# Performance work log

Measured on AMD Instinct MI355X. Metric: run time of the kernel, lower is better.

The kernel has to match this reference:

```python
import jax, jax.numpy as jnp
import numpy as np

INPUT_DIM = 1024
BOTTLENECK = 256
NUM_Q = 8
CODEBOOK = 1024
COMMIT_W = 0.25

def setup_inputs() -> dict:
    key = jax.random.key(0)
    ks = jax.random.split(key, 10)
    s_in = 1.0 / np.sqrt(INPUT_DIM)
    s_bn = 1.0 / np.sqrt(BOTTLENECK)
    return {
        'x': jax.random.normal(ks[0], (8, 2048, INPUT_DIM), jnp.float32),
        'W_e1': jax.random.uniform(ks[1], (INPUT_DIM, INPUT_DIM), jnp.float32, -s_in, s_in),
        'b_e1': jnp.zeros((INPUT_DIM,), jnp.float32),
        'W_e2': jax.random.uniform(ks[2], (INPUT_DIM, BOTTLENECK), jnp.float32, -s_in, s_in),
        'b_e2': jnp.zeros((BOTTLENECK,), jnp.float32),
        'codebooks': jax.random.normal(ks[3], (NUM_Q, CODEBOOK, BOTTLENECK), jnp.float32),
        'W_d1': jax.random.uniform(ks[4], (BOTTLENECK, INPUT_DIM), jnp.float32, -s_bn, s_bn),
        'b_d1': jnp.zeros((INPUT_DIM,), jnp.float32),
        'W_d2': jax.random.uniform(ks[5], (INPUT_DIM, INPUT_DIM), jnp.float32, -s_in, s_in),
        'b_d2': jnp.zeros((INPUT_DIM,), jnp.float32),
    }

def _gelu(x):
    return jax.nn.gelu(x, approximate=False)  # torch nn.GELU default = exact erf

def _rvq(z_flat, codebooks):
    # z_flat: [N, D]; codebooks: [Q, K, D]
    def step(res, cb):
        # squared L2 distances via expansion: [N, K]
        d2 = (jnp.sum(res * res, -1, keepdims=True)
              - 2.0 * res @ cb.T
              + jnp.sum(cb * cb, -1))
        idx = jnp.argmin(d2, axis=-1)                      # [N]
        q = jax.lax.stop_gradient(jnp.take(cb, idx, 0))    # [N, D] (EMA codebook: no grad)
        closs = jnp.mean((res - q) ** 2)
        return res - q, (idx, q, closs)
    _, (indices, qs, closses) = jax.lax.scan(step, z_flat, codebooks)
    q_total = jnp.sum(qs, axis=0)
    # straight-through estimator
    quantized = z_flat + jax.lax.stop_gradient(q_total - z_flat)
    commitment = COMMIT_W * jnp.mean(closses)
    return quantized, indices, commitment

def reference(x, W_e1, b_e1, W_e2, b_e2, codebooks, W_d1, b_d1, W_d2, b_d2):
    lead = x.shape[:-1]
    z = _gelu(x @ W_e1 + b_e1) @ W_e2 + b_e2               # [..., BOTTLENECK]
    zf = z.reshape(-1, BOTTLENECK)
    qf, indices, commitment = _rvq(zf, codebooks)
    quantized = qf.reshape(*lead, BOTTLENECK)
    indices = indices.reshape(NUM_Q, *lead)
    reconstructed = _gelu(quantized @ W_d1 + b_d1) @ W_d2 + b_d2
    return z, quantized, indices, reconstructed, commitment
```

## Files before the change

### kernel.cpp

```cpp
#include <hip/hip_runtime.h>
#include <math.h>

#define NROWS 16384
#define DIN   1024
#define DBN   256
#define NQ    8
#define NCODE 1024
#define MARGIN 2.0f

#define OFF_Z    0
#define OFF_Q    4194304
#define OFF_IDX  8388608
#define OFF_REC  8519680
#define OFF_COM  25296896

typedef __attribute__((ext_vector_type(8))) short short8v;
typedef __attribute__((ext_vector_type(4))) float f32x4;

__device__ __forceinline__ float gelu_f(float x) {
  return 0.5f * x * (1.0f + erff(x * 0.70710678118654752440f));
}

__device__ __forceinline__ ushort f2b(float x) {
  unsigned u = __float_as_uint(x);
  unsigned r = u + 0x7FFF + ((u >> 16) & 1);
  return (ushort)(r >> 16);
}
__device__ __forceinline__ float b2f(ushort u) {
  return __uint_as_float((unsigned)u << 16);
}
__device__ __forceinline__ void split3(float v, ushort& s1, ushort& s2, ushort& s3) {
  s1 = f2b(v);
  const float r1 = v - b2f(s1);
  s2 = f2b(r1);
  s3 = f2b(r1 - b2f(s2));
}

template<bool GELU, bool TWO>
__global__ __launch_bounds__(256) void gemm6(
    const float* __restrict__ Af,
    const ushort* __restrict__ B1, const ushort* __restrict__ B2,
    const ushort* __restrict__ B3,
    const float* __restrict__ bias,
    float* __restrict__ C0, float* __restrict__ C1,
    int N, int K)
{
  __shared__ char lds[49152];
  char* ldsA1 = lds;
  char* ldsA2 = lds + 8192;
  char* ldsA3 = lds + 16384;
  char* ldsB1 = lds + 24576;
  char* ldsB2 = lds + 32768;
  char* ldsB3 = lds + 40960;
  const int tid = threadIdx.x;
  const int bm = blockIdx.x * 128;
  const int bn = blockIdx.y * 128;
  const int lane = tid & 63;
  const int wid = tid >> 6;
  const int wr = wid >> 1, wc = wid & 1;

  const int srow = tid >> 1;
  const int skh  = tid & 1;
  const float* Ap  = Af + (size_t)(bm + srow) * K + skh * 16;
  const ushort* Bp1 = B1 + (size_t)(bn + srow) * K + skh * 16;
  const ushort* Bp2 = B2 + (size_t)(bn + srow) * K + skh * 16;
  const ushort* Bp3 = B3 + (size_t)(bn + srow) * K + skh * 16;
  const int sswz = (srow & 3) << 4;
  const int sbase = srow * 64 + skh * 32;

  f32x4 acc[4][4];
  #pragma unroll
  for (int m = 0; m < 4; ++m)
    #pragma unroll
    for (int n = 0; n < 4; ++n) acc[m][n] = (f32x4)0.f;

  const int nt = K >> 5;
  for (int t = 0; t < nt; ++t) {
    const int k0 = t << 5;
    __syncthreads();
    #pragma unroll
    for (int jf = 0; jf < 4; ++jf) {
      const float4 v = *(const float4*)(Ap + k0 + jf * 4);
      ushort4 h, md, l;
      split3(v.x, h.x, md.x, l.x);
      split3(v.y, h.y, md.y, l.y);
      split3(v.z, h.z, md.z, l.z);
      split3(v.w, h.w, md.w, l.w);
      const int off = (sbase + jf * 8) ^ sswz;
      *(ushort4*)(ldsA1 + off) = h;
      *(ushort4*)(ldsA2 + off) = md;
      *(ushort4*)(ldsA3 + off) = l;
    }
    #pragma unroll
    for (int j = 0; j < 2; ++j) {
      const int off = (sbase + j * 16) ^ sswz;
      *(uint4*)(ldsB1 + off) = *(const uint4*)(Bp1 + k0 + j * 8);
      *(uint4*)(ldsB2 + off) = *(const uint4*)(Bp2 + k0 + j * 8);
      *(uint4*)(ldsB3 + off) = *(const uint4*)(Bp3 + k0 + j * 8);
    }
    __syncthreads();

    short8v a1[4], a2[4], a3[4], b1[4], b2[4], b3[4];
    #pragma unroll
    for (int m = 0; m < 4; ++m) {
      const int row = wr * 64 + m * 16 + (lane & 15);
      const int off = (row * 64 + ((lane >> 4) << 4)) ^ ((row & 3) << 4);
      a1[m] = *(const short8v*)(ldsA1 + off);
      a2[m] = *(const short8v*)(ldsA2 + off);
      a3[m] = *(const short8v*)(ldsA3 + off);
    }
    #pragma unroll
    for (int n = 0; n < 4; ++n) {
      const int row = wc * 64 + n * 16 + (lane & 15);
      const int off = (row * 64 + ((lane >> 4) << 4)) ^ ((row & 3) << 4);
      b1[n] = *(const short8v*)(ldsB1 + off);
      b2[n] = *(const short8v*)(ldsB2 + off);
      b3[n] = *(const short8v*)(ldsB3 + off);
    }
    #pragma unroll
    for (int m = 0; m < 4; ++m)
      #pragma unroll
      for (int n = 0; n < 4; ++n) {
        f32x4 a = acc[m][n];
        a = __builtin_amdgcn_mfma_f32_16x16x32_bf16(a3[m], b1[n], a, 0, 0, 0);
        a = __builtin_amdgcn_mfma_f32_16x16x32_bf16(a1[m], b3[n], a, 0, 0, 0);
        a = __builtin_amdgcn_mfma_f32_16x16x32_bf16(a2[m], b2[n], a, 0, 0, 0);
        a = __builtin_amdgcn_mfma_f32_16x16x32_bf16(a2[m], b1[n], a, 0, 0, 0);
        a = __builtin_amdgcn_mfma_f32_16x16x32_bf16(a1[m], b2[n], a, 0, 0, 0);
        a = __builtin_amdgcn_mfma_f32_16x16x32_bf16(a1[m], b1[n], a, 0, 0, 0);
        acc[m][n] = a;
      }
  }

  #pragma unroll
  for (int n = 0; n < 4; ++n) {
    const int col = bn + wc * 64 + n * 16 + (lane & 15);
    const float bb = bias[col];
    #pragma unroll
    for (int m = 0; m < 4; ++m) {
      const int row0 = bm + wr * 64 + m * 16 + ((lane >> 4) << 2);
      #pragma unroll
      for (int r = 0; r < 4; ++r) {
        float v = acc[m][n][r] + bb;
        if (GELU) v = gelu_f(v);
        C0[(size_t)(row0 + r) * N + col] = v;
        if (TWO) C1[(size_t)(row0 + r) * N + col] = v;
      }
    }
  }
}

__device__ __forceinline__ void mm_core(
    const ushort* __restrict__ A, const ushort* __restrict__ B,
    int K, int bm, int bn, char* lds, f32x4 acc[4][4])
{
  char* ldsA = lds;
  char* ldsB = lds + 16384;
  const int tid = threadIdx.x;
  const int lane = tid & 63;
  const int wid = tid >> 6;
  const int wr = wid >> 1, wc = wid & 1;

  #pragma unroll
  for (int m = 0; m < 4; ++m)
    #pragma unroll
    for (int n = 0; n < 4; ++n) acc[m][n] = (f32x4)0.f;

  const int nt = K >> 6;
  for (int t = 0; t < nt; ++t) {
    const int k0 = t << 6;
    __syncthreads();
    #pragma unroll
    for (int c = 0; c < 4; ++c) {
      const int id = c * 256 + tid;
      const int row = id >> 3, k8 = id & 7;
      const uint4 va = *(const uint4*)(A + (size_t)(bm + row) * K + k0 + k8 * 8);
      const uint4 vb = *(const uint4*)(B + (size_t)(bn + row) * K + k0 + k8 * 8);
      const int off = (row * 128 + k8 * 16) ^ ((row & 7) << 4);
      *(uint4*)(ldsA + off) = va;
      *(uint4*)(ldsB + off) = vb;
    }
    __syncthreads();
    #pragma unroll
    for (int kk = 0; kk < 2; ++kk) {
      short8v af[4], bfr[4];
      #pragma unroll
      for (int m = 0; m < 4; ++m) {
        const int row = wr * 64 + m * 16 + (lane & 15);
        af[m] = *(const short8v*)(ldsA +
            ((row * 128 + kk * 64 + ((lane >> 4) << 4)) ^ ((row & 7) << 4)));
      }
      #pragma unroll
      for (int n = 0; n < 4; ++n) {
        const int row = wc * 64 + n * 16 + (lane & 15);
        bfr[n] = *(const short8v*)(ldsB +
            ((row * 128 + kk * 64 + ((lane >> 4) << 4)) ^ ((row & 7) << 4)));
      }
      #pragma unroll
      for (int m = 0; m < 4; ++m)
        #pragma unroll
        for (int n = 0; n < 4; ++n)
          acc[m][n] = __builtin_amdgcn_mfma_f32_16x16x32_bf16(
              af[m], bfr[n], acc[m][n], 0, 0, 0);
    }
  }
}

__global__ __launch_bounds__(256) void rvq_screen(
    const ushort* __restrict__ resb, const ushort* __restrict__ cbb,
    const float* __restrict__ cnorm, _Float16* __restrict__ D)
{
  __shared__ char lds[32768];
  f32x4 acc[4][4];
  const int bm = blockIdx.x * 128, bn = blockIdx.y * 128;
  mm_core(resb, cbb, DBN, bm, bn, lds, acc);
  const int lane = threadIdx.x & 63;
  const int wid = threadIdx.x >> 6;
  const int wr = wid >> 1, wc = wid & 1;
  #pragma unroll
  for (int n = 0; n < 4; ++n) {
    const int col = bn + wc * 64 + n * 16 + (lane & 15);
    const float cn = cnorm[col];
    #pragma unroll
    for (int m = 0; m < 4; ++m) {
      const int row0 = bm + wr * 64 + m * 16 + ((lane >> 4) << 2);
      #pragma unroll
      for (int r = 0; r < 4; ++r)
        D[(size_t)(row0 + r) * NCODE + col] = (_Float16)(cn - 2.0f * acc[m][n][r]);
    }
  }
}

template<bool GELU, bool OUTF>
__global__ __launch_bounds__(256) void gemm_bf16(
    const ushort* __restrict__ A, const ushort* __restrict__ Bt,
    const float* __restrict__ bias, float* __restrict__ Cf,
    ushort* __restrict__ Cb, int N, int K)
{
  __shared__ char lds[32768];
  f32x4 acc[4][4];
  const int bm = blockIdx.x * 128, bn = blockIdx.y * 128;
  mm_core(A, Bt, K, bm, bn, lds, acc);
  const int lane = threadIdx.x & 63;
  const int wid = threadIdx.x >> 6;
  const int wr = wid >> 1, wc = wid & 1;
  #pragma unroll
  for (int n = 0; n < 4; ++n) {
    const int col = bn + wc * 64 + n * 16 + (lane & 15);
    const float bb = bias[col];
    #pragma unroll
    for (int m = 0; m < 4; ++m) {
      const int row0 = bm + wr * 64 + m * 16 + ((lane >> 4) << 2);
      #pragma unroll
      for (int r = 0; r < 4; ++r) {
        float v = acc[m][n][r] + bb;
        if (GELU) v = gelu_f(v);
        if (OUTF) Cf[(size_t)(row0 + r) * N + col] = v;
        else      Cb[(size_t)(row0 + r) * N + col] = f2b(v);
      }
    }
  }
}

__global__ __launch_bounds__(256) void cnorm_kernel(
    const float* __restrict__ cb, float* __restrict__ cnorm)
{
  const int code = blockIdx.x * 4 + (threadIdx.x >> 6);
  const int lane = threadIdx.x & 63;
  float4 v = *(const float4*)(cb + (size_t)code * DBN + lane * 4);
  float s = v.x * v.x + v.y * v.y + v.z * v.z + v.w * v.w;
  #pragma unroll
  for (int o = 32; o > 0; o >>= 1) s += __shfl_down(s, o, 64);
  if (lane == 0) cnorm[code] = s;
}

__global__ __launch_bounds__(256) void rvq_rescore(
    const _Float16* __restrict__ D, const float* __restrict__ cb_s,
    const float* __restrict__ cnorm_s,
    float* __restrict__ res, ushort* __restrict__ resb,
    float* __restrict__ idx_out, float* __restrict__ closs_part)
{
  __shared__ int cnt[4];
  __shared__ ushort cand[4][128];
  __shared__ float wsum[4];
  const int w = threadIdx.x >> 6, lane = threadIdx.x & 63;
  const int row = blockIdx.x * 4 + w;
  if (lane == 0) cnt[w] = 0;

  union H8 { uint4 u; _Float16 h[8]; };
  const _Float16* Dr = D + (size_t)row * NCODE + lane * 16;
  H8 a0, a1;
  a0.u = *(const uint4*)(Dr);
  a1.u = *(const uint4*)(Dr + 8);
  float dv[16];
  #pragma unroll
  for (int i = 0; i < 8; ++i) { dv[i] = (float)a0.h[i]; dv[8 + i] = (float)a1.h[i]; }

  float mn = dv[0];
  #pragma unroll
  for (int i = 1; i < 16; ++i) mn = fminf(mn, dv[i]);
  #pragma unroll
  for (int o = 32; o > 0; o >>= 1) mn = fminf(mn, __shfl_xor(mn, o, 64));
  const float thr = mn + MARGIN;

  #pragma unroll
  for (int i = 0; i < 16; ++i)
    if (dv[i] < thr) {
      int p = atomicAdd(&cnt[w], 1);
      if (p < 128) cand[w][p] = (ushort)(lane * 16 + i);
    }
  const int ncand = min(cnt[w], 128);

  const float4 r4 = *(const float4*)(res + (size_t)row * DBN + lane * 4);
  float bestv = INFINITY; int besti = 0x7fffffff;
  for (int c = 0; c < ncand; ++c) {
    const int code = cand[w][c];
    const float4 c4 = *(const float4*)(cb_s + (size_t)code * DBN + lane * 4);
    float d = r4.x * c4.x + r4.y * c4.y + r4.z * c4.z + r4.w * c4.w;
    #pragma unroll
    for (int o = 32; o > 0; o >>= 1) d += __shfl_xor(d, o, 64);
    const float ex = cnorm_s[code] - 2.0f * d;
    if (ex < bestv || (ex == bestv && code < besti)) { bestv = ex; besti = code; }
  }

  const float4 q4 = *(const float4*)(cb_s + (size_t)besti * DBN + lane * 4);
  float4 n4;
  n4.x = r4.x - q4.x; n4.y = r4.y - q4.y; n4.z = r4.z - q4.z; n4.w = r4.w - q4.w;
  *(float4*)(res + (size_t)row * DBN + lane * 4) = n4;
  ushort4 nb;
  nb.x = f2b(n4.x); nb.y = f2b(n4.y); nb.z = f2b(n4.z); nb.w = f2b(n4.w);
  *(ushort4*)(resb + (size_t)row * DBN + lane * 4) = nb;

  float s = n4.x * n4.x + n4.y * n4.y + n4.z * n4.z + n4.w * n4.w;
  #pragma unroll
  for (int o = 32; o > 0; o >>= 1) s += __shfl_xor(s, o, 64);
  if (lane == 0) { wsum[w] = s; idx_out[row] = (float)besti; }
  __syncthreads();
  if (threadIdx.x == 0)
    closs_part[blockIdx.x] = wsum[0] + wsum[1] + wsum[2] + wsum[3];
}

__global__ __launch_bounds__(256) void qfix_gather(
    const float* __restrict__ z, const float* __restrict__ idxf,
    const float* __restrict__ cb, float* __restrict__ q, ushort* __restrict__ qb)
{
  const int w = threadIdx.x >> 6, lane = threadIdx.x & 63;
  const int row = blockIdx.x * 4 + w;
  float4 a; a.x = 0.f; a.y = 0.f; a.z = 0.f; a.w = 0.f;
  #pragma unroll
  for (int s = 0; s < NQ; ++s) {
    const int ix = (int)idxf[(size_t)s * NROWS + row];
    const float4 c4 = *(const float4*)(cb + ((size_t)s * NCODE + ix) * DBN + lane * 4);
    a.x += c4.x; a.y += c4.y; a.z += c4.z; a.w += c4.w;
  }
  const float4 z4 = *(const float4*)(z + (size_t)row * DBN + lane * 4);
  float4 qv;
  qv.x = z4.x + (a.x - z4.x); qv.y = z4.y + (a.y - z4.y);
  qv.z = z4.z + (a.z - z4.z); qv.w = z4.w + (a.w - z4.w);
  *(float4*)(q + (size_t)row * DBN + lane * 4) = qv;
  ushort4 qb4;
  qb4.x = f2b(qv.x); qb4.y = f2b(qv.y); qb4.z = f2b(qv.z); qb4.w = f2b(qv.w);
  *(ushort4*)(qb + (size_t)row * DBN + lane * 4) = qb4;
}

__global__ __launch_bounds__(256) void conv_flat(
    const float* __restrict__ in, ushort* __restrict__ out, int n4)
{
  const int i = blockIdx.x * 256 + threadIdx.x;
  if (i >= n4) return;
  const float4 v = *(const float4*)(in + (size_t)i * 4);
  ushort4 o;
  o.x = f2b(v.x); o.y = f2b(v.y); o.z = f2b(v.z); o.w = f2b(v.w);
  *(ushort4*)(out + (size_t)i * 4) = o;
}

__global__ __launch_bounds__(256) void convT(
    const float* __restrict__ in, ushort* __restrict__ out, int K, int N)
{
  __shared__ float t[32][33];
  const int k0 = blockIdx.x * 32, n0 = blockIdx.y * 32;
  const int tx = threadIdx.x & 31, ty = threadIdx.x >> 5;
  #pragma unroll
  for (int i = 0; i < 32; i += 8)
    t[ty + i][tx] = in[(size_t)(k0 + ty + i) * N + n0 + tx];
  __syncthreads();
  #pragma unroll
  for (int i = 0; i < 32; i += 8)
    out[(size_t)(n0 + ty + i) * K + k0 + tx] = f2b(t[tx][ty + i]);
}

__global__ __launch_bounds__(256) void convT_split3(
    const float* __restrict__ in, ushort* __restrict__ o1,
    ushort* __restrict__ o2, ushort* __restrict__ o3, int K, int N)
{
  __shared__ float t[32][33];
  const int k0 = blockIdx.x * 32, n0 = blockIdx.y * 32;
  const int tx = threadIdx.x & 31, ty = threadIdx.x >> 5;
  #pragma unroll
  for (int i = 0; i < 32; i += 8)
    t[ty + i][tx] = in[(size_t)(k0 + ty + i) * N + n0 + tx];
  __syncthreads();
  #pragma unroll
  for (int i = 0; i < 32; i += 8) {
    const float v = t[tx][ty + i];
    ushort s1, s2, s3;
    split3(v, s1, s2, s3);
    const size_t o = (size_t)(n0 + ty + i) * K + k0 + tx;
    o1[o] = s1; o2[o] = s2; o3[o] = s3;
  }
}

__global__ __launch_bounds__(256) void commit_kernel(
    const float* __restrict__ parts, float* __restrict__ out)
{
  __shared__ float sm[256];
  float s = 0.f;
  for (int i = threadIdx.x; i < NQ * 4096; i += 256) s += parts[i];
  sm[threadIdx.x] = s;
  __syncthreads();
  for (int st = 128; st > 0; st >>= 1) {
    if (threadIdx.x < st) sm[threadIdx.x] += sm[threadIdx.x + st];
    __syncthreads();
  }
  if (threadIdx.x == 0)
    out[0] = 0.25f * sm[0] / (8.0f * 4194304.0f);
}

extern "C" void kernel_launch(void* const* d_in, const int* in_sizes, int n_in,
                              void* d_out, int out_size, void* d_ws, size_t ws_size,
                              hipStream_t stream) {
  (void)in_sizes; (void)n_in; (void)out_size; (void)ws_size;
  const float* x    = (const float*)d_in[0];
  const float* W_e1 = (const float*)d_in[1];
  const float* b_e1 = (const float*)d_in[2];
  const float* W_e2 = (const float*)d_in[3];
  const float* b_e2 = (const float*)d_in[4];
  const float* cb   = (const float*)d_in[5];
  const float* W_d1 = (const float*)d_in[6];
  const float* b_d1 = (const float*)d_in[7];
  const float* W_d2 = (const float*)d_in[8];
  const float* b_d2 = (const float*)d_in[9];

  float* out = (float*)d_out;
  float* z_out   = out + OFF_Z;
  float* q_out   = out + OFF_Q;
  float* idx_out = out + OFF_IDX;
  float* rec_out = out + OFF_REC;
  float* com_out = out + OFF_COM;

  float* ws      = (float*)d_ws;
  float* hidden  = ws;
  float* res     = ws + 16777216;
  float* cnorm   = ws + 20971520;
  float* closs   = ws + 20979712;
  ushort* wtail  = (ushort*)(ws + 21012480);
  ushort* We2T1  = wtail;
  ushort* We2T2  = wtail + 262144;
  ushort* We2T3  = wtail + 524288;
  ushort* Wd1T   = wtail + 786432;
  ushort* Wd2T   = wtail + 1048576;

  ushort* resu   = (ushort*)res;
  ushort* We1T1  = resu;
  ushort* We1T2  = resu + 1048576;
  ushort* We1T3  = resu + 2097152;

  ushort* hregion = (ushort*)d_ws;
  _Float16* Dmat = (_Float16*)hregion;
  ushort* resb   = hregion + 16777216;
  ushort* cbb    = hregion + 20971520;
  ushort* qb     = hregion + 20971520;
  ushort* hidb   = hregion;

  cnorm_kernel<<<2048, 256, 0, stream>>>(cb, cnorm);
  convT_split3<<<dim3(32, 32), 256, 0, stream>>>(W_e1, We1T1, We1T2, We1T3, DIN, DIN);
  convT_split3<<<dim3(32, 8),  256, 0, stream>>>(W_e2, We2T1, We2T2, We2T3, DIN, DBN);
  convT<<<dim3(8, 32),  256, 0, stream>>>(W_d1, Wd1T, DBN, DIN);
  convT<<<dim3(32, 32), 256, 0, stream>>>(W_d2, Wd2T, DIN, DIN);

  gemm6<true,  false><<<dim3(128, 8), 256, 0, stream>>>(
      x, We1T1, We1T2, We1T3, b_e1, hidden, nullptr, DIN, DIN);
  gemm6<false, true ><<<dim3(128, 2), 256, 0, stream>>>(
      hidden, We2T1, We2T2, We2T3, b_e2, z_out, res, DBN, DIN);

  conv_flat<<<4096, 256, 0, stream>>>(res, resb, 1048576);
  conv_flat<<<2048, 256, 0, stream>>>(cb, cbb, 524288);

  for (int s = 0; s < NQ; ++s) {
    rvq_screen<<<dim3(128, 8), 256, 0, stream>>>(
        resb, cbb + (size_t)s * NCODE * DBN, cnorm + s * NCODE, Dmat);
    rvq_rescore<<<4096, 256, 0, stream>>>(
        Dmat, cb + (size_t)s * NCODE * DBN, cnorm + s * NCODE,
        res, resb, idx_out + (size_t)s * NROWS, closs + s * 4096);
  }

  qfix_gather<<<4096, 256, 0, stream>>>(z_out, idx_out, cb, q_out, qb);

  gemm_bf16<true,  false><<<dim3(128, 8), 256, 0, stream>>>(qb, Wd1T, b_d1, nullptr, hidb, DIN, DBN);
  gemm_bf16<false, true ><<<dim3(128, 8), 256, 0, stream>>>(hidb, Wd2T, b_d2, rec_out, nullptr, DIN, DIN);

  commit_kernel<<<1, 256, 0, stream>>>(closs, com_out);
}
```

Baseline: 706.7 us.

## Interleave split-bf16 LDS tiles, narrow second encoder GEMM tile, fuse bf16 residual output

The three bf16 split planes of A and B now sit interleaved per row in one LDS buffer with an 8-way XOR swizzle. The A split is done on 16 contiguous floats and written as 16-byte vectors. The second encoder GEMM is templated to a 64-column tile so it launches 512 blocks instead of 256, which gives more parallelism on that small-N GEMM. It also writes the bf16 copy of the residual directly, which removes a separate conversion kernel. The trade-off is more A reloads for the narrow tile and extra stores in the epilogue.

```diff
diff --git a/kernel.cpp b/kernel.cpp
--- a/kernel.cpp
+++ b/kernel.cpp
@@ -33,108 +33,126 @@
   s1 = f2b(v);
   const float r1 = v - b2f(s1);
   s2 = f2b(r1);
-  s3 = f2b(r1 - b2f(s2));
-}
-
-template<bool GELU, bool TWO>
+  const float r2 = r1 - b2f(s2);
+  s3 = f2b(r2);
+}
+
+template<bool GELU, int NB, int OUT>
 __global__ __launch_bounds__(256) void gemm6(
     const float* __restrict__ Af,
     const ushort* __restrict__ B1, const ushort* __restrict__ B2,
     const ushort* __restrict__ B3,
     const float* __restrict__ bias,
-    float* __restrict__ C0, float* __restrict__ C1,
+    float* __restrict__ C0, float* __restrict__ C1, ushort* __restrict__ Ob,
     int N, int K)
 {
-  __shared__ char lds[49152];
-  char* ldsA1 = lds;
-  char* ldsA2 = lds + 8192;
-  char* ldsA3 = lds + 16384;
-  char* ldsB1 = lds + 24576;
-  char* ldsB2 = lds + 32768;
-  char* ldsB3 = lds + 40960;
+  constexpr int BN = NB * 32;
+  __shared__ char lds[24576 + BN * 192];
+  char* ldsA = lds;
+  char* ldsB = lds + 24576;
   const int tid = threadIdx.x;
   const int bm = blockIdx.x * 128;
-  const int bn = blockIdx.y * 128;
+  const int bn = blockIdx.y * BN;
   const int lane = tid & 63;
   const int wid = tid >> 6;
   const int wr = wid >> 1, wc = wid & 1;
 
-  const int srow = tid >> 1;
-  const int skh  = tid & 1;
-  const float* Ap  = Af + (size_t)(bm + srow) * K + skh * 16;
-  const ushort* Bp1 = B1 + (size_t)(bn + srow) * K + skh * 16;
-  const ushort* Bp2 = B2 + (size_t)(bn + srow) * K + skh * 16;
-  const ushort* Bp3 = B3 + (size_t)(bn + srow) * K + skh * 16;
-  const int sswz = (srow & 3) << 4;
-  const int sbase = srow * 64 + skh * 32;
-
-  f32x4 acc[4][4];
+  const int srow = tid >> 1, skh = tid & 1;
+  const float* Ap = Af + (size_t)(bm + srow) * K + skh * 16;
+  const int abase = srow * 192;
+  const int aswz = (srow & 7) << 4;
+
+  f32x4 acc[4][NB];
   #pragma unroll
   for (int m = 0; m < 4; ++m)
     #pragma unroll
-    for (int n = 0; n < 4; ++n) acc[m][n] = (f32x4)0.f;
+    for (int n = 0; n < NB; ++n) acc[m][n] = (f32x4)0.f;
+
+  union U8 { ushort u[8]; short8v v; };
 
   const int nt = K >> 5;
   for (int t = 0; t < nt; ++t) {
     const int k0 = t << 5;
     __syncthreads();
-    #pragma unroll
-    for (int jf = 0; jf < 4; ++jf) {
-      const float4 v = *(const float4*)(Ap + k0 + jf * 4);
-      ushort4 h, md, l;
-      split3(v.x, h.x, md.x, l.x);
-      split3(v.y, h.y, md.y, l.y);
-      split3(v.z, h.z, md.z, l.z);
-      split3(v.w, h.w, md.w, l.w);
-      const int off = (sbase + jf * 8) ^ sswz;
-      *(ushort4*)(ldsA1 + off) = h;
-      *(ushort4*)(ldsA2 + off) = md;
-      *(ushort4*)(ldsA3 + off) = l;
-    }
-    #pragma unroll
-    for (int j = 0; j < 2; ++j) {
-      const int off = (sbase + j * 16) ^ sswz;
-      *(uint4*)(ldsB1 + off) = *(const uint4*)(Bp1 + k0 + j * 8);
-      *(uint4*)(ldsB2 + off) = *(const uint4*)(Bp2 + k0 + j * 8);
-      *(uint4*)(ldsB3 + off) = *(const uint4*)(Bp3 + k0 + j * 8);
+    float av[16];
+    *(float4*)&av[0]  = *(const float4*)(Ap + k0);
+    *(float4*)&av[4]  = *(const float4*)(Ap + k0 + 4);
+    *(float4*)&av[8]  = *(const float4*)(Ap + k0 + 8);
+    *(float4*)&av[12] = *(const float4*)(Ap + k0 + 12);
+    U8 p1[2], p2[2], p3[2];
+    #pragma unroll
+    for (int i = 0; i < 16; ++i) {
+      ushort s1, s2, s3;
+      split3(av[i], s1, s2, s3);
+      p1[i >> 3].u[i & 7] = s1;
+      p2[i >> 3].u[i & 7] = s2;
+      p3[i >> 3].u[i & 7] = s3;
+    }
+    #pragma unroll
+    for (int h2 = 0; h2 < 2; ++h2) {
+      const int kb = skh * 32 + h2 * 16;
+      *(short8v*)(ldsA + ((abase + 0   + kb) ^ aswz)) = p1[h2].v;
+      *(short8v*)(ldsA + ((abase + 64  + kb) ^ aswz)) = p2[h2].v;
+      *(short8v*)(ldsA + ((abase + 128 + kb) ^ aswz)) = p3[h2].v;
+    }
+    if (NB == 4) {
+      const int br = tid >> 1, bk = tid & 1;
+      const size_t g = (size_t)(bn + br) * K + k0 + bk * 16;
+      const int bb = br * 192, bswz = (br & 7) << 4;
+      #pragma unroll
+      for (int h2 = 0; h2 < 2; ++h2) {
+        const int kb = bk * 32 + h2 * 16;
+        *(uint4*)(ldsB + ((bb + 0   + kb) ^ bswz)) = *(const uint4*)(B1 + g + h2 * 8);
+        *(uint4*)(ldsB + ((bb + 64  + kb) ^ bswz)) = *(const uint4*)(B2 + g + h2 * 8);
+        *(uint4*)(ldsB + ((bb + 128 + kb) ^ bswz)) = *(const uint4*)(B3 + g + h2 * 8);
+      }
+    } else {
+      const int br = tid >> 2, bk = tid & 3;
+      const size_t g = (size_t)(bn + br) * K + k0 + bk * 8;
+      const int bb = br * 192, bswz = (br & 7) << 4;
+      const int kb = bk * 16;
+      *(uint4*)(ldsB + ((bb + 0   + kb) ^ bswz)) = *(const uint4*)(B1 + g);
+      *(uint4*)(ldsB + ((bb + 64  + kb) ^ bswz)) = *(const uint4*)(B2 + g);
+      *(uint4*)(ldsB + ((bb + 128 + kb) ^ bswz)) = *(const uint4*)(B3 + g);
     }
     __syncthreads();
 
-    short8v a1[4], a2[4], a3[4], b1[4], b2[4], b3[4];
+    const int kq = (lane >> 4) << 4;
+    short8v a1[4], a2[4], a3[4], b1v[NB], b2v[NB], b3v[NB];
     #pragma unroll
     for (int m = 0; m < 4; ++m) {
       const int row = wr * 64 + m * 16 + (lane & 15);
-      const int off = (row * 64 + ((lane >> 4) << 4)) ^ ((row & 3) << 4);
-      a1[m] = *(const short8v*)(ldsA1 + off);
-      a2[m] = *(const short8v*)(ldsA2 + off);
-      a3[m] = *(const short8v*)(ldsA3 + off);
-    }
-    #pragma unroll
-    for (int n = 0; n < 4; ++n) {
-      const int row = wc * 64 + n * 16 + (lane & 15);
-      const int off = (row * 64 + ((lane >> 4) << 4)) ^ ((row & 3) << 4);
-      b1[n] = *(const short8v*)(ldsB1 + off);
-      b2[n] = *(const short8v*)(ldsB2 + off);
-      b3[n] = *(const short8v*)(ldsB3 + off);
+      const int base = row * 192, swz = (row & 7) << 4;
+      a1[m] = *(const short8v*)(ldsA + ((base + 0   + kq) ^ swz));
+      a2[m] = *(const short8v*)(ldsA + ((base + 64  + kq) ^ swz));
+      a3[m] = *(const short8v*)(ldsA + ((base + 128 + kq) ^ swz));
+    }
+    #pragma unroll
+    for (int n = 0; n < NB; ++n) {
+      const int row = wc * (NB * 16) + n * 16 + (lane & 15);
+      const int base = row * 192, swz = (row & 7) << 4;
+      b1v[n] = *(const short8v*)(ldsB + ((base + 0   + kq) ^ swz));
+      b2v[n] = *(const short8v*)(ldsB + ((base + 64  + kq) ^ swz));
+      b3v[n] = *(const short8v*)(ldsB + ((base + 128 + kq) ^ swz));
     }
     #pragma unroll
     for (int m = 0; m < 4; ++m)
       #pragma unroll
-      for (int n = 0; n < 4; ++n) {
+      for (int n = 0; n < NB; ++n) {
         f32x4 a = acc[m][n];
-        a = __builtin_amdgcn_mfma_f32_16x16x32_bf16(a3[m], b1[n], a, 0, 0, 0);
-        a = __builtin_amdgcn_mfma_f32_16x16x32_bf16(a1[m], b3[n], a, 0, 0, 0);
-        a = __builtin_amdgcn_mfma_f32_16x16x32_bf16(a2[m], b2[n], a, 0, 0, 0);
-        a = __builtin_amdgcn_mfma_f32_16x16x32_bf16(a2[m], b1[n], a, 0, 0, 0);
-        a = __builtin_amdgcn_mfma_f32_16x16x32_bf16(a1[m], b2[n], a, 0, 0, 0);
-        a = __builtin_amdgcn_mfma_f32_16x16x32_bf16(a1[m], b1[n], a, 0, 0, 0);
+        a = __builtin_amdgcn_mfma_f32_16x16x32_bf16(a3[m], b1v[n], a, 0, 0, 0);
+        a = __builtin_amdgcn_mfma_f32_16x16x32_bf16(a1[m], b3v[n], a, 0, 0, 0);
+        a = __builtin_amdgcn_mfma_f32_16x16x32_bf16(a2[m], b2v[n], a, 0, 0, 0);
+        a = __builtin_amdgcn_mfma_f32_16x16x32_bf16(a2[m], b1v[n], a, 0, 0, 0);
+        a = __builtin_amdgcn_mfma_f32_16x16x32_bf16(a1[m], b2v[n], a, 0, 0, 0);
+        a = __builtin_amdgcn_mfma_f32_16x16x32_bf16(a1[m], b1v[n], a, 0, 0, 0);
         acc[m][n] = a;
       }
   }
 
   #pragma unroll
-  for (int n = 0; n < 4; ++n) {
-    const int col = bn + wc * 64 + n * 16 + (lane & 15);
+  for (int n = 0; n < NB; ++n) {
+    const int col = bn + wc * (NB * 16) + n * 16 + (lane & 15);
     const float bb = bias[col];
     #pragma unroll
     for (int m = 0; m < 4; ++m) {
@@ -144,7 +162,10 @@
         float v = acc[m][n][r] + bb;
         if (GELU) v = gelu_f(v);
         C0[(size_t)(row0 + r) * N + col] = v;
-        if (TWO) C1[(size_t)(row0 + r) * N + col] = v;
+        if (OUT == 1) {
+          C1[(size_t)(row0 + r) * N + col] = v;
+          Ob[(size_t)(row0 + r) * N + col] = f2b(v);
+        }
       }
     }
   }
@@ -478,12 +499,11 @@
   convT<<<dim3(8, 32),  256, 0, stream>>>(W_d1, Wd1T, DBN, DIN);
   convT<<<dim3(32, 32), 256, 0, stream>>>(W_d2, Wd2T, DIN, DIN);
 
-  gemm6<true,  false><<<dim3(128, 8), 256, 0, stream>>>(
-      x, We1T1, We1T2, We1T3, b_e1, hidden, nullptr, DIN, DIN);
-  gemm6<false, true ><<<dim3(128, 2), 256, 0, stream>>>(
-      hidden, We2T1, We2T2, We2T3, b_e2, z_out, res, DBN, DIN);
-
-  conv_flat<<<4096, 256, 0, stream>>>(res, resb, 1048576);
+  gemm6<true,  4, 0><<<dim3(128, 8), 256, 0, stream>>>(
+      x, We1T1, We1T2, We1T3, b_e1, hidden, nullptr, nullptr, DIN, DIN);
+  gemm6<false, 2, 1><<<dim3(128, 4), 256, 0, stream>>>(
+      hidden, We2T1, We2T2, We2T3, b_e2, z_out, res, resb, DBN, DIN);
+
   conv_flat<<<2048, 256, 0, stream>>>(cb, cbb, 524288);
 
   for (int s = 0; s < NQ; ++s) {
```

New measurement: 683.3 us. 1.03x faster.
